# Optimization experiments

Hardware: AMD Instinct MI355X
Metric: run time of the kernel (lower is better)

## Reference

```python
import jax, jax.numpy as jnp
import numpy as np

D_MODEL = 256
D_INNER = 512
NHEADS = 8
HEADDIM = 64
NGROUPS = 1
D_DIST = 4
LOG_SCALE = 512.0
MAX_VALUE = 4.0
NUM_POINTS = 10
EPS = 1e-5


def roty(t):
    c, s = jnp.cos(t), jnp.sin(t)
    z, o = jnp.zeros_like(t), jnp.ones_like(t)
    r0 = jnp.stack([c, z, s], -1)
    r1 = jnp.stack([z, o, z], -1)
    r2 = jnp.stack([-s, z, c], -1)
    return jnp.stack([r0, r1, r2], -2)


def box_corners(center, size, angle):
    # flip_axis_to_camera: (x, -z, y)
    cam_c = jnp.stack([center[..., 0], -center[..., 2], center[..., 1]], -1)
    R = roty(angle)  # (B,K,3,3)
    sx = jnp.array([1, 1, -1, -1, 1, 1, -1, -1], jnp.float32)
    sy = jnp.array([1, 1, 1, 1, -1, -1, -1, -1], jnp.float32)
    sz = jnp.array([1, -1, -1, 1, 1, -1, -1, 1], jnp.float32)
    l, w, h = size[..., 0:1], size[..., 1:2], size[..., 2:3]
    local = jnp.stack([l * sx / 2, h * sy / 2, w * sz / 2], -1)  # (B,K,8,3)
    cam = jnp.einsum('bkcj,bkij->bkci', local, R) + cam_c[..., None, :]
    # camera -> lidar: (x, z, -y)
    return jnp.stack([cam[..., 0], cam[..., 2], -cam[..., 1]], -1)


def trilinear_sample(table, g):
    # table (P,P,P,C); g (N,3) normalized coords (gx,gy,gz); gx->axis2, gy->axis1, gz->axis0
    # replicates F.grid_sample(mode='bilinear', align_corners=False, padding_mode='zeros')
    P = table.shape[0]
    pix = ((g + 1.0) * P - 1.0) * 0.5
    k, j, i = pix[:, 0], pix[:, 1], pix[:, 2]
    i0f, j0f, k0f = jnp.floor(i), jnp.floor(j), jnp.floor(k)
    wi, wj, wk = i - i0f, j - j0f, k - k0f
    i0, j0, k0 = i0f.astype(jnp.int32), j0f.astype(jnp.int32), k0f.astype(jnp.int32)
    out = jnp.zeros((g.shape[0], table.shape[-1]), table.dtype)
    for a in (0, 1):
        for b in (0, 1):
            for c in (0, 1):
                ii, jj, kk = i0 + a, j0 + b, k0 + c
                valid = (ii >= 0) & (ii < P) & (jj >= 0) & (jj < P) & (kk >= 0) & (kk < P)
                v = table[jnp.clip(ii, 0, P - 1), jnp.clip(jj, 0, P - 1), jnp.clip(kk, 0, P - 1)]
                w = (wi if a else 1 - wi) * (wj if b else 1 - wj) * (wk if c else 1 - wk)
                out = out + jnp.where(valid, w, 0.0)[:, None] * v
    return out


def box_dist(key_xyz, query_xyz, query_size, query_angle, w1, b1, w2):
    B, K = query_xyz.shape[:2]
    L = key_xyz.shape[1]
    corners = jax.lax.stop_gradient(box_corners(query_xyz, query_size, query_angle))
    d = corners.reshape(B, K * 8, 3)[:, :, None, :] - key_xyz[:, None, :, :]  # (B,K*8,L,3)
    d = jnp.stack([d[..., 0], -d[..., 2], d[..., 1]], -1)
    R = roty(jnp.tile(query_angle, (1, 8)))  # matches torch .repeat((1,8)) ordering (bug-faithful)
    d = jnp.einsum('bqlj,bqjk->bqlk', d, R)
    d = jnp.stack([d[..., 0], d[..., 2], -d[..., 1]], -1)
    d = jnp.sign(d) * jnp.log2(jnp.abs(d) * LOG_SCALE + 1.0) / np.float32(np.log2(8.0))
    g = (d / MAX_VALUE).reshape(-1, 3)
    lin = jnp.linspace(-MAX_VALUE, MAX_VALUE, NUM_POINTS, dtype=jnp.float32)
    coords = jnp.stack(jnp.meshgrid(lin, lin, lin, indexing='ij'), -1)  # (P,P,P,3)
    table = jnp.maximum(coords @ w1.T + b1, 0.0) @ w2.T  # cpb MLP -> (P,P,P,4)
    samp = trilinear_sample(table, g).reshape(B, K, 8, L, D_DIST)
    return samp.sum(axis=2).transpose(0, 2, 1, 3)  # (B,L,K,4)


def dwconv7(x, w, b):
    # x (B,L,C), depthwise conv1d k=7 pad=3
    y = jax.lax.conv_general_dilated(jnp.swapaxes(x, 1, 2), w, (1,), [(3, 3)],
                                     dimension_numbers=('NCH', 'OIH', 'NCH'),
                                     feature_group_count=w.shape[0])
    return jnp.swapaxes(y + b[None, :, None], 1, 2)


def issm_scan(x, Bm, Cm, dt, A, h0):
    # x (B,L,H,hd), Bm/Cm (B,L,K), dt (B,L,K,H), h0 (B,H,hd,K); state index = query axis K
    dA = jnp.exp(dt * A)          # (B,L,K,H)
    dB = dt * Bm[..., None]       # (B,L,K,H)
    xs = (jnp.moveaxis(x, 1, 0), jnp.moveaxis(dA, 1, 0), jnp.moveaxis(dB, 1, 0), jnp.moveaxis(Cm, 1, 0))

    def step(h, inp):
        x_t, dA_t, dB_t, C_t = inp
        h = h * jnp.swapaxes(dA_t, 1, 2)[:, :, None, :] + x_t[..., None] * jnp.swapaxes(dB_t, 1, 2)[:, :, None, :]
        return h, jnp.einsum('bhdk,bk->bhd', h, C_t)

    hT, ys = jax.lax.scan(step, h0, xs)
    return jnp.moveaxis(ys, 0, 1), hT


def _forward(in_key, in_query, key_xyz, query_xyz, query_size, query_angle, Wkey, conv_w, conv_b, convb_w, convb_b, Wq, Wbc, Wdt, dt_bias, A_log, Dp, Wok, Woq, key_norm_w, ln_w, ln_b, cpb_w1, cpb_b1, cpb_w2):
    B, L, _ = in_key.shape
    K = in_query.shape[1]
    zxbcdt = in_key @ Wkey.T
    z = zxbcdt[..., :D_INNER]
    xbc = zxbcdt[..., D_INNER:2 * D_INNER + 2 * NGROUPS]
    dt_k = zxbcdt[..., 2 * D_INNER + 2 * NGROUPS:]
    xbc_f = jax.nn.silu(dwconv7(xbc, conv_w, conv_b))
    x = xbc_f[..., :D_INNER].reshape(B, L, NHEADS, HEADDIM)
    b_bias = xbc_f[..., D_INNER:D_INNER + NGROUPS]
    c_bias = xbc_f[..., D_INNER + NGROUPS:]
    xbc_b = jax.nn.silu(dwconv7(xbc_f, convb_w, convb_b))
    x_b = xbc_b[..., :D_INNER].reshape(B, L, NHEADS, HEADDIM)
    bb_b = xbc_b[..., D_INNER:D_INNER + NGROUPS]
    cb_b = xbc_b[..., D_INNER + NGROUPS:]
    dist = box_dist(key_xyz, query_xyz, query_size, query_angle, cpb_w1, cpb_b1, cpb_w2)  # (B,L,K,4)
    bc = dist @ Wbc.T  # (B,L,K,2*ngroups)
    Bm0, Cm0 = bc[..., 0], bc[..., 1]
    dt = jax.nn.softplus(dist @ Wdt.T + dt_k[:, :, None, :] + dt_bias)  # (B,L,K,H)
    A = -jnp.exp(A_log)
    h0 = (in_query @ Wq.T).reshape(B, K, NHEADS, HEADDIM).transpose(0, 2, 3, 1)  # (B,H,hd,K)
    y_f, h_f = issm_scan(x, Bm0 + b_bias, Cm0 + c_bias, dt, A, h0)
    rev = lambda a: jnp.flip(a, axis=1)
    y_b, h_b = issm_scan(rev(x_b), rev(Bm0 + bb_b), rev(Cm0 + cb_b), rev(dt), A, h0)
    y = y_f + rev(y_b) + Dp[None, None, :, None] * x
    yk = y.reshape(B, L, D_INNER)
    gated = yk * jax.nn.silu(z)
    gated = gated * jax.lax.rsqrt(jnp.mean(gated * gated, -1, keepdims=True) + EPS) * key_norm_w
    out_key = gated @ Wok.T
    state = (0.5 * (h_f + h_b)).transpose(0, 3, 1, 2).reshape(B, K, D_INNER)
    mu = jnp.mean(state, -1, keepdims=True)
    var = jnp.mean((state - mu) ** 2, -1, keepdims=True)
    out_query = (((state - mu) * jax.lax.rsqrt(var + EPS)) * ln_w + ln_b) @ Woq.T
    return out_key, out_query


def setup_inputs():
    key = jax.random.key(0)
    ks = jax.random.split(key, 24)
    B, L, K = 2, 1024, 128
    D, DI, H, G = D_MODEL, D_INNER, NHEADS, NGROUPS
    CC = DI + 2 * G
    n = jax.random.normal
    inp = {}
    inp['in_key'] = n(ks[0], (B, L, D), jnp.float32)
    inp['in_query'] = n(ks[1], (B, K, D), jnp.float32)
    inp['key_xyz'] = jax.random.uniform(ks[2], (B, L, 3))
    inp['query_xyz'] = jax.random.uniform(ks[3], (B, K, 3))
    inp['query_size'] = jax.random.uniform(ks[4], (B, K, 3)) + 0.1
    inp['query_angle'] = jax.random.uniform(ks[5], (B, K)) * 2.0 * np.float32(np.pi)
    inp['Wkey'] = n(ks[6], (2 * DI + 2 * G + H, D)) * 0.02
    inp['conv_w'] = n(ks[7], (CC, 1, 7)) * 0.1
    inp['conv_b'] = jnp.zeros((CC,))
    inp['convb_w'] = n(ks[8], (CC, 1, 7)) * 0.1
    inp['convb_b'] = jnp.zeros((CC,))
    inp['Wq'] = n(ks[9], (DI, D)) * 0.02
    inp['Wbc'] = n(ks[10], (2 * G, D_DIST)) * 0.1
    inp['Wdt'] = n(ks[11], (H, D_DIST)) * 0.1
    dt = jnp.exp(jax.random.uniform(ks[12], (H,)) * (np.float32(np.log(0.1)) - np.float32(np.log(1e-4))) + np.float32(np.log(1e-4)))
    inp['dt_bias'] = dt + jnp.log(-jnp.expm1(-dt))
    inp['A_log'] = jnp.log(jax.random.uniform(ks[13], (H,), minval=1.0, maxval=16.0))
    inp['Dp'] = jnp.ones((H,))
    inp['Wok'] = n(ks[14], (D, DI)) * 0.02
    inp['Woq'] = n(ks[15], (D, DI)) * 0.02
    inp['key_norm_w'] = jnp.ones((DI,))
    inp['ln_w'] = jnp.ones((DI,))
    inp['ln_b'] = jnp.zeros((DI,))
    inp['cpb_w1'] = n(ks[16], (128, 3)) * 0.1
    inp['cpb_b1'] = jnp.zeros((128,))
    inp['cpb_w2'] = n(ks[17], (D_DIST, 128)) * 0.1
    return inp


def reference(in_key, in_query, key_xyz, query_xyz, query_size, query_angle, Wkey, conv_w, conv_b, convb_w, convb_b, Wq, Wbc, Wdt, dt_bias, A_log, Dp, Wok, Woq, key_norm_w, ln_w, ln_b, cpb_w1, cpb_b1, cpb_w2):
    return _forward(in_key, in_query, key_xyz, query_xyz, query_size, query_angle, Wkey, conv_w, conv_b, convb_w, convb_b, Wq, Wbc, Wdt, dt_bias, A_log, Dp, Wok, Woq, key_norm_w, ln_w, ln_b, cpb_w1, cpb_b1, cpb_w2)
```

## Files before the change

kernel.cpp:

```cpp
#include <hip/hip_runtime.h>
#include <math.h>

#define B_ 2
#define L_ 1024
#define K_ 128
#define DM 256
#define DI 512
#define NH 8
#define HD 64
#define CC 514
#define ZCOLS 1034
#define NC 16
#define TC 64

__device__ __forceinline__ float wave_sum(float v) {
    v += __shfl_xor(v, 1);  v += __shfl_xor(v, 2);  v += __shfl_xor(v, 4);
    v += __shfl_xor(v, 8);  v += __shfl_xor(v, 16); v += __shfl_xor(v, 32);
    return v;
}

__device__ __forceinline__ float dpp_row_reduce16(float v) {
    int t;
    t = __builtin_amdgcn_update_dpp(0, __float_as_int(v), 0x128, 0xF, 0xF, true);
    v += __int_as_float(t);
    t = __builtin_amdgcn_update_dpp(0, __float_as_int(v), 0x124, 0xF, 0xF, true);
    v += __int_as_float(t);
    t = __builtin_amdgcn_update_dpp(0, __float_as_int(v), 0x122, 0xF, 0xF, true);
    v += __int_as_float(t);
    t = __builtin_amdgcn_update_dpp(0, __float_as_int(v), 0x121, 0xF, 0xF, true);
    v += __int_as_float(t);
    return v;
}

__device__ __forceinline__ float silu_f(float x) {
    return x / (1.f + expf(-x));
}

__device__ void gemm_dev(const float* __restrict__ A, const float* __restrict__ Bm,
                         float* __restrict__ C, int M, int N, int K, int bm, int bn) {
    __shared__ float As[2][16][68];
    __shared__ float Bs[2][16][68];
    const int tid = threadIdx.x;
    const int sr = tid >> 2;
    const int sk = (tid & 3) * 4;
    const int tx = tid & 15, ty = tid >> 4;
    const int NT = K >> 4;
    const float* Arow = A + (size_t)(bm + sr) * K + sk;
    const float* Brow = Bm + (size_t)(bn + sr) * K + sk;
    const bool bok = (bn + sr) < N;

    float4 av = *(const float4*)Arow;
    float4 bv = bok ? *(const float4*)Brow : make_float4(0.f, 0.f, 0.f, 0.f);
    As[0][sk + 0][sr] = av.x; As[0][sk + 1][sr] = av.y;
    As[0][sk + 2][sr] = av.z; As[0][sk + 3][sr] = av.w;
    Bs[0][sk + 0][sr] = bv.x; Bs[0][sk + 1][sr] = bv.y;
    Bs[0][sk + 2][sr] = bv.z; Bs[0][sk + 3][sr] = bv.w;
    __syncthreads();

    float acc[4][4] = {};
    for (int t = 0; t < NT; ++t) {
        if (t + 1 < NT) {
            av = *(const float4*)(Arow + (t + 1) * 16);
            bv = bok ? *(const float4*)(Brow + (t + 1) * 16) : make_float4(0.f, 0.f, 0.f, 0.f);
        }
        const int bi = t & 1;
#pragma unroll
        for (int kk = 0; kk < 16; ++kk) {
            float4 a = *(const float4*)&As[bi][kk][ty * 4];
            float4 b = *(const float4*)&Bs[bi][kk][tx * 4];
            acc[0][0] = fmaf(a.x, b.x, acc[0][0]); acc[0][1] = fmaf(a.x, b.y, acc[0][1]);
            acc[0][2] = fmaf(a.x, b.z, acc[0][2]); acc[0][3] = fmaf(a.x, b.w, acc[0][3]);
            acc[1][0] = fmaf(a.y, b.x, acc[1][0]); acc[1][1] = fmaf(a.y, b.y, acc[1][1]);
            acc[1][2] = fmaf(a.y, b.z, acc[1][2]); acc[1][3] = fmaf(a.y, b.w, acc[1][3]);
            acc[2][0] = fmaf(a.z, b.x, acc[2][0]); acc[2][1] = fmaf(a.z, b.y, acc[2][1]);
            acc[2][2] = fmaf(a.z, b.z, acc[2][2]); acc[2][3] = fmaf(a.z, b.w, acc[2][3]);
            acc[3][0] = fmaf(a.w, b.x, acc[3][0]); acc[3][1] = fmaf(a.w, b.y, acc[3][1]);
            acc[3][2] = fmaf(a.w, b.z, acc[3][2]); acc[3][3] = fmaf(a.w, b.w, acc[3][3]);
        }
        if (t + 1 < NT) {
            const int ni = (t + 1) & 1;
            As[ni][sk + 0][sr] = av.x; As[ni][sk + 1][sr] = av.y;
            As[ni][sk + 2][sr] = av.z; As[ni][sk + 3][sr] = av.w;
            Bs[ni][sk + 0][sr] = bv.x; Bs[ni][sk + 1][sr] = bv.y;
            Bs[ni][sk + 2][sr] = bv.z; Bs[ni][sk + 3][sr] = bv.w;
        }
        __syncthreads();
    }
#pragma unroll
    for (int i = 0; i < 4; ++i) {
        int m = bm + ty * 4 + i;
        int n0 = bn + tx * 4;
        if (n0 + 3 < N) {
            float* cp = &C[(size_t)m * N + n0];
            *(float2*)cp = make_float2(acc[i][0], acc[i][1]);
            *(float2*)(cp + 2) = make_float2(acc[i][2], acc[i][3]);
        } else {
#pragma unroll
            for (int j = 0; j < 4; ++j)
                if (n0 + j < N) C[(size_t)m * N + n0 + j] = acc[i][j];
        }
    }
}

__global__ __launch_bounds__(256, 4) void front_k(
    const float* __restrict__ in_key, const float* __restrict__ Wkey, float* __restrict__ zx,
    const float* __restrict__ in_query, const float* __restrict__ Wq, float* __restrict__ h0b,
    const float* __restrict__ qxyz, const float* __restrict__ qsize,
    const float* __restrict__ qang, const float* __restrict__ w1,
    const float* __restrict__ b1, const float* __restrict__ w2,
    float* __restrict__ cb, float* __restrict__ tbl) {
    int bid = blockIdx.x, tid = threadIdx.x;
    if (bid < 544) {
        gemm_dev(in_key, Wkey, zx, 2048, ZCOLS, 256, (bid & 31) * 64, (bid >> 5) * 64);
    } else if (bid < 576) {
        int r = bid - 544;
        gemm_dev(in_query, Wq, h0b, 256, 512, 256, (r & 3) * 64, (r >> 2) * 64);
    } else if (bid < 584) {
        int idx = (bid - 576) * 256 + tid;
        int b = idx >> 10;
        int q = idx & 1023;
        int k = q >> 3;
        int c = q & 7;
        const float sx[8] = {1, 1, -1, -1, 1, 1, -1, -1};
        const float sy[8] = {1, 1, 1, 1, -1, -1, -1, -1};
        const float sz[8] = {1, -1, -1, 1, 1, -1, -1, 1};
        float cx = qxyz[(b * K_ + k) * 3 + 0];
        float cy = qxyz[(b * K_ + k) * 3 + 1];
        float cz = qxyz[(b * K_ + k) * 3 + 2];
        float lv = qsize[(b * K_ + k) * 3 + 0];
        float wv = qsize[(b * K_ + k) * 3 + 1];
        float hv = qsize[(b * K_ + k) * 3 + 2];
        float ang = qang[b * K_ + k];
        float ca = cosf(ang), sa = sinf(ang);
        float ccx = cx, ccy = -cz, ccz = cy;
        float l0 = lv * sx[c] * 0.5f;
        float l1 = hv * sy[c] * 0.5f;
        float l2 = wv * sz[c] * 0.5f;
        float m0 = ca * l0 + sa * l2 + ccx;
        float m1 = l1 + ccy;
        float m2 = -sa * l0 + ca * l2 + ccz;
        float angr = qang[b * K_ + (q & (K_ - 1))];
        float4* o = (float4*)(cb + (size_t)idx * 8);
        o[0] = make_float4(m0, m2, -m1, cosf(angr));
        o[1] = make_float4(sinf(angr), 0.f, 0.f, 0.f);
    } else {
        int p = (bid - 584) * 256 + tid;
        if (p >= 1000) return;
        int i = p / 100, j = (p / 10) % 10, k = p % 10;
        float c0 = (8.f / 9.f) * i - 4.f;
        float c1 = (8.f / 9.f) * j - 4.f;
        float c2 = (8.f / 9.f) * k - 4.f;
        float a0 = 0.f, a1 = 0.f, a2 = 0.f, a3 = 0.f;
        for (int m = 0; m < 128; ++m) {
            float t = fmaf(c0, w1[m * 3 + 0], fmaf(c1, w1[m * 3 + 1], fmaf(c2, w1[m * 3 + 2], b1[m])));
            t = fmaxf(t, 0.f);
            a0 = fmaf(t, w2[m], a0);
            a1 = fmaf(t, w2[128 + m], a1);
            a2 = fmaf(t, w2[256 + m], a2);
            a3 = fmaf(t, w2[384 + m], a3);
        }
        tbl[p * 4 + 0] = a0; tbl[p * 4 + 1] = a1;
        tbl[p * 4 + 2] = a2; tbl[p * 4 + 3] = a3;
    }
}

__global__ void dwconv_silu(const float* __restrict__ xin, int in_stride, int in_off,
                            const float* __restrict__ w, const float* __restrict__ bias,
                            float* __restrict__ out) {
    int c = blockIdx.y * blockDim.x + threadIdx.x;
    if (c >= CC) return;
    int row0 = blockIdx.x * 2;
    int l0 = row0 & (L_ - 1);
    const float* xr = xin + (size_t)row0 * in_stride + in_off + c;
    float Lv[8];
#pragma unroll
    for (int i = 0; i < 8; ++i) {
        int ll = l0 + i - 3;
        Lv[i] = (ll >= 0 && ll < L_) ? xr[(ptrdiff_t)(i - 3) * in_stride] : 0.f;
    }
    float acc0 = bias[c], acc1 = bias[c];
#pragma unroll
    for (int j = 0; j < 7; ++j) {
        float wj = w[c * 7 + j];
        acc0 = fmaf(Lv[j], wj, acc0);
        acc1 = fmaf(Lv[j + 1], wj, acc1);
    }
    out[(size_t)row0 * CC + c] = silu_f(acc0);
    out[(size_t)(row0 + 1) * CC + c] = silu_f(acc1);
}

__global__ __launch_bounds__(128) void geo_k(
    const float* __restrict__ kxyz, const float* __restrict__ cb,
    const float* __restrict__ tbl, const float* __restrict__ zx,
    const float* __restrict__ xf, const float* __restrict__ xb,
    const float* __restrict__ wbc, const float* __restrict__ wdt,
    const float* __restrict__ dtb, const float* __restrict__ alog,
    float* __restrict__ dA, float* __restrict__ dBf, float* __restrict__ dBb,
    float* __restrict__ Cf, float* __restrict__ Cb) {
    __shared__ float t_s[4000];
    int row = blockIdx.x;
    int b = row >> 10;
    int l = row & 1023;
    int k = threadIdx.x;
    for (int i = threadIdx.x; i < 4000; i += 128) t_s[i] = tbl[i];
    __syncthreads();
    float kx = kxyz[(size_t)row * 3 + 0];
    float ky = kxyz[(size_t)row * 3 + 1];
    float kz = kxyz[(size_t)row * 3 + 2];
    float acc0 = 0.f, acc1 = 0.f, acc2 = 0.f, acc3 = 0.f;
#pragma unroll
    for (int c = 0; c < 8; ++c) {
        int q = k * 8 + c;
        const float4* p = (const float4*)(cb + (size_t)(b * 1024 + q) * 8);
        float4 v0 = p[0], v1 = p[1];
        float d0 = v0.x - kx, d1 = v0.y - ky, d2 = v0.z - kz;
        float rc = v0.w, rs = v1.x;
        float e0 = d0, e1 = -d2, e2 = d1;
        float f0 = rc * e0 - rs * e2;
        float f1 = e1;
        float f2 = rs * e0 + rc * e2;
        float g0 = f0, g1 = f2, g2 = -f1;
        g0 = copysignf(log2f(fabsf(g0) * 512.f + 1.f) * (1.f / 12.f), g0);
        g1 = copysignf(log2f(fabsf(g1) * 512.f + 1.f) * (1.f / 12.f), g1);
        g2 = copysignf(log2f(fabsf(g2) * 512.f + 1.f) * (1.f / 12.f), g2);
        float iq = 5.f * g2 + 4.5f;
        float jq = 5.f * g1 + 4.5f;
        float kq = 5.f * g0 + 4.5f;
        float i0f = floorf(iq), j0f = floorf(jq), k0f = floorf(kq);
        float wi = iq - i0f, wj = jq - j0f, wk = kq - k0f;
        int i0 = (int)i0f, j0 = (int)j0f, k0 = (int)k0f;
#pragma unroll
        for (int a = 0; a < 2; ++a) {
#pragma unroll
            for (int bb = 0; bb < 2; ++bb) {
#pragma unroll
                for (int cc = 0; cc < 2; ++cc) {
                    int ii = i0 + a, jj = j0 + bb, kk = k0 + cc;
                    if ((unsigned)ii < 10u && (unsigned)jj < 10u && (unsigned)kk < 10u) {
                        float wgt = (a ? wi : 1.f - wi) * (bb ? wj : 1.f - wj) * (cc ? wk : 1.f - wk);
                        const float* tp = &t_s[((ii * 10 + jj) * 10 + kk) * 4];
                        acc0 = fmaf(wgt, tp[0], acc0);
                        acc1 = fmaf(wgt, tp[1], acc1);
                        acc2 = fmaf(wgt, tp[2], acc2);
                        acc3 = fmaf(wgt, tp[3], acc3);
                    }
                }
            }
        }
    }
    float B0 = acc0 * wbc[0] + acc1 * wbc[1] + acc2 * wbc[2] + acc3 * wbc[3];
    float C0 = acc0 * wbc[4] + acc1 * wbc[5] + acc2 * wbc[6] + acc3 * wbc[7];
    float bbf = xf[(size_t)row * CC + 512], cbf = xf[(size_t)row * CC + 513];
    float bbb = xb[(size_t)row * CC + 512], cbb = xb[(size_t)row * CC + 513];
    Cf[(size_t)row * K_ + k] = C0 + cbf;
    Cb[(size_t)row * K_ + k] = C0 + cbb;
    float Bf = B0 + bbf, Bb = B0 + bbb;
#pragma unroll
    for (int hh = 0; hh < NH; ++hh) {
        float s = acc0 * wdt[hh * 4 + 0] + acc1 * wdt[hh * 4 + 1] +
                  acc2 * wdt[hh * 4 + 2] + acc3 * wdt[hh * 4 + 3];
        s += zx[(size_t)row * ZCOLS + 1026 + hh] + dtb[hh];
        float dtv = (s > 20.f) ? s : log1pf(expf(s));
        float Av = -expf(alog[hh]);
        size_t o = ((size_t)(b * NH + hh) * L_ + l) * K_ + k;
        dA[o] = expf(dtv * Av);
        dBf[o] = dtv * Bf;
        dBb[o] = dtv * Bb;
    }
}

__global__ __launch_bounds__(256) void scan_part6(
    const float* __restrict__ dA, const float* __restrict__ dBf, const float* __restrict__ dBb,
    const float* __restrict__ Cf, const float* __restrict__ Cb,
    const float* __restrict__ xf, const float* __restrict__ xb,
    float* __restrict__ Sbuf, float* __restrict__ Pbuf,
    float* __restrict__ yf, float* __restrict__ yb) {
    __shared__ float lds[2][3584];
    int bid = blockIdx.x;
    int c = bid & 15;
    int hh = (bid >> 4) & 7;
    int b = (bid >> 7) & 1;
    int dir = bid >> 8;
    int tid = threadIdx.x;
    int lane = tid & 63;
    int w = tid >> 6;
    int dg = lane >> 4, kg = lane & 15;
    int dloc = w * 4 + dg;
    int klo = kg * 4, khi = 64 + kg * 4;

    const float* Bsrc = dir ? dBb : dBf;
    const float* Csrc = dir ? Cb : Cf;
    const float* Xsrc = dir ? xb : xf;
    float* Ydst = dir ? yb : yf;
    int t0 = dir ? (L_ - 1 - c * TC) : c * TC;
    int stp = dir ? -1 : 1;

    const float* Abase = dA + ((size_t)(b * NH + hh) * L_) * K_;
    const float* Bbase = Bsrc + ((size_t)(b * NH + hh) * L_) * K_;
    const float* Cbase = Csrc + ((size_t)b * L_) * K_;
    const float* Xbase = Xsrc + ((size_t)b * L_) * CC + hh * HD;

    const bool hasx = (tid < 128);

    auto gaddr = [&](int v, int tb) -> const float* {
        if (v < 768) {
            int r = (v >> 5) & 7;
            int c4 = v & 31;
            int l = t0 + stp * (tb + r);
            const float* base = (v < 256) ? Abase : ((v < 512) ? Bbase : Cbase);
            return base + (size_t)l * K_ + c4 * 4;
        } else {
            int vv = v - 768;
            int r = vv >> 4, c4 = vv & 15;
            int l = t0 + stp * (tb + r);
            return Xbase + (size_t)l * CC + c4 * 4;
        }
    };

    float hA[8] = {0, 0, 0, 0, 0, 0, 0, 0};
    float hB[8] = {0, 0, 0, 0, 0, 0, 0, 0};
    float hC[8] = {0, 0, 0, 0, 0, 0, 0, 0};
    float hD[8] = {0, 0, 0, 0, 0, 0, 0, 0};
    float cum[8] = {1, 1, 1, 1, 1, 1, 1, 1};

    float4 rA = *(const float4*)gaddr(tid, 0);
    float4 rB = *(const float4*)gaddr(256 + tid, 0);
    float4 rC = *(const float4*)gaddr(512 + tid, 0);
    float4 rX = hasx ? *(const float4*)gaddr(768 + tid, 0) : make_float4(0, 0, 0, 0);
    *(float4*)&lds[0][4 * tid] = rA;
    *(float4*)&lds[0][1024 + 4 * tid] = rB;
    *(float4*)&lds[0][2048 + 4 * tid] = rC;
    if (hasx) *(float4*)&lds[0][3072 + 4 * tid] = rX;
    __syncthreads();

    float* pY = Ydst + ((size_t)(b * L_ + t0)) * DI + hh * HD + dloc;
    const ptrdiff_t dY = (ptrdiff_t)stp * DI;

    for (int it = 0; it < TC / 8; ++it) {
        int tb = it * 8;
        if (it < TC / 8 - 1) {
            rA = *(const float4*)gaddr(tid, tb + 8);
            rB = *(const float4*)gaddr(256 + tid, tb + 8);
            rC = *(const float4*)gaddr(512 + tid, tb + 8);
            if (hasx) rX = *(const float4*)gaddr(768 + tid, tb + 8);
        }
        const float* Lb = lds[it & 1];
        float4 aC0 = *(const float4*)&Lb[klo];
        float4 aC1 = *(const float4*)&Lb[khi];
        float4 bC0 = *(const float4*)&Lb[1024 + klo];
        float4 bC1 = *(const float4*)&Lb[1024 + khi];
        float4 cC0 = *(const float4*)&Lb[2048 + klo];
        float4 cC1 = *(const float4*)&Lb[2048 + khi];
        float x0 = Lb[3072 + dloc];
        float x1 = Lb[3072 + 16 + dloc];
        float x2 = Lb[3072 + 32 + dloc];
        float x3 = Lb[3072 + 48 + dloc];
        float4 aN0 = *(const float4*)&Lb[128 + klo];
        float4 aN1 = *(const float4*)&Lb[128 + khi];
        float4 bN0 = *(const float4*)&Lb[1024 + 128 + klo];
        float4 bN1 = *(const float4*)&Lb[1024 + 128 + khi];
#pragma unroll
        for (int st = 0; st < 8; ++st) {
            float4 aF0, aF1, bF0, bF1, cN0, cN1;
            float nx0 = 0.f, nx1 = 0.f, nx2 = 0.f, nx3 = 0.f;
            if (st < 6) {
                int o = (st + 2) * 128;
                aF0 = *(const float4*)&Lb[o + klo];
                aF1 = *(const float4*)&Lb[o + khi];
                bF0 = *(const float4*)&Lb[1024 + o + klo];
                bF1 = *(const float4*)&Lb[1024 + o + khi];
            }
            if (st < 7) {
                int o = (st + 1) * 128;
                cN0 = *(const float4*)&Lb[2048 + o + klo];
                cN1 = *(const float4*)&Lb[2048 + o + khi];
                int xo = 3072 + (st + 1) * 64 + dloc;
                nx0 = Lb[xo]; nx1 = Lb[xo + 16]; nx2 = Lb[xo + 32]; nx3 = Lb[xo + 48];
            }
            cum[0] *= aC0.x; cum[1] *= aC0.y; cum[2] *= aC0.z; cum[3] *= aC0.w;
            cum[4] *= aC1.x; cum[5] *= aC1.y; cum[6] *= aC1.z; cum[7] *= aC1.w;
            float u0, u1, u2, u3;
            hA[0] = fmaf(hA[0], aC0.x, x0 * bC0.x); u0 = hA[0] * cC0.x;
            hA[1] = fmaf(hA[1], aC0.y, x0 * bC0.y); u1 = hA[1] * cC0.y;
            hA[2] = fmaf(hA[2], aC0.z, x0 * bC0.z); u2 = hA[2] * cC0.z;
            hA[3] = fmaf(hA[3], aC0.w, x0 * bC0.w); u3 = hA[3] * cC0.w;
            hA[4] = fmaf(hA[4], aC1.x, x0 * bC1.x); u0 = fmaf(hA[4], cC1.x, u0);
            hA[5] = fmaf(hA[5], aC1.y, x0 * bC1.y); u1 = fmaf(hA[5], cC1.y, u1);
            hA[6] = fmaf(hA[6], aC1.z, x0 * bC1.z); u2 = fmaf(hA[6], cC1.z, u2);
            hA[7] = fmaf(hA[7], aC1.w, x0 * bC1.w); u3 = fmaf(hA[7], cC1.w, u3);
            float rrA = dpp_row_reduce16((u0 + u1) + (u2 + u3));
            hB[0] = fmaf(hB[0], aC0.x, x1 * bC0.x); u0 = hB[0] * cC0.x;
            hB[1] = fmaf(hB[1], aC0.y, x1 * bC0.y); u1 = hB[1] * cC0.y;
            hB[2] = fmaf(hB[2], aC0.z, x1 * bC0.z); u2 = hB[2] * cC0.z;
            hB[3] = fmaf(hB[3], aC0.w, x1 * bC0.w); u3 = hB[3] * cC0.w;
            hB[4] = fmaf(hB[4], aC1.x, x1 * bC1.x); u0 = fmaf(hB[4], cC1.x, u0);
            hB[5] = fmaf(hB[5], aC1.y, x1 * bC1.y); u1 = fmaf(hB[5], cC1.y, u1);
            hB[6] = fmaf(hB[6], aC1.z, x1 * bC1.z); u2 = fmaf(hB[6], cC1.z, u2);
            hB[7] = fmaf(hB[7], aC1.w, x1 * bC1.w); u3 = fmaf(hB[7], cC1.w, u3);
            float rrB = dpp_row_reduce16((u0 + u1) + (u2 + u3));
            hC[0] = fmaf(hC[0], aC0.x, x2 * bC0.x); u0 = hC[0] * cC0.x;
            hC[1] = fmaf(hC[1], aC0.y, x2 * bC0.y); u1 = hC[1] * cC0.y;
            hC[2] = fmaf(hC[2], aC0.z, x2 * bC0.z); u2 = hC[2] * cC0.z;
            hC[3] = fmaf(hC[3], aC0.w, x2 * bC0.w); u3 = hC[3] * cC0.w;
            hC[4] = fmaf(hC[4], aC1.x, x2 * bC1.x); u0 = fmaf(hC[4], cC1.x, u0);
            hC[5] = fmaf(hC[5], aC1.y, x2 * bC1.y); u1 = fmaf(hC[5], cC1.y, u1);
            hC[6] = fmaf(hC[6], aC1.z, x2 * bC1.z); u2 = fmaf(hC[6], cC1.z, u2);
            hC[7] = fmaf(hC[7], aC1.w, x2 * bC1.w); u3 = fmaf(hC[7], cC1.w, u3);
            float rrC = dpp_row_reduce16((u0 + u1) + (u2 + u3));
            hD[0] = fmaf(hD[0], aC0.x, x3 * bC0.x); u0 = hD[0] * cC0.x;
            hD[1] = fmaf(hD[1], aC0.y, x3 * bC0.y); u1 = hD[1] * cC0.y;
            hD[2] = fmaf(hD[2], aC0.z, x3 * bC0.z); u2 = hD[2] * cC0.z;
            hD[3] = fmaf(hD[3], aC0.w, x3 * bC0.w); u3 = hD[3] * cC0.w;
            hD[4] = fmaf(hD[4], aC1.x, x3 * bC1.x); u0 = fmaf(hD[4], cC1.x, u0);
            hD[5] = fmaf(hD[5], aC1.y, x3 * bC1.y); u1 = fmaf(hD[5], cC1.y, u1);
            hD[6] = fmaf(hD[6], aC1.z, x3 * bC1.z); u2 = fmaf(hD[6], cC1.z, u2);
            hD[7] = fmaf(hD[7], aC1.w, x3 * bC1.w); u3 = fmaf(hD[7], cC1.w, u3);
            float rrD = dpp_row_reduce16((u0 + u1) + (u2 + u3));
            if (kg == 0) { pY[0] = rrA; pY[16] = rrB; pY[32] = rrC; pY[48] = rrD; }
            pY += dY;
            if (st < 7) {
                aC0 = aN0; aC1 = aN1; bC0 = bN0; bC1 = bN1;
                cC0 = cN0; cC1 = cN1;
                x0 = nx0; x1 = nx1; x2 = nx2; x3 = nx3;
                if (st < 6) { aN0 = aF0; aN1 = aF1; bN0 = bF0; bN1 = bF1; }
            }
        }
        if (it < TC / 8 - 1) {
            *(float4*)&lds[(it + 1) & 1][4 * tid] = rA;
            *(float4*)&lds[(it + 1) & 1][1024 + 4 * tid] = rB;
            *(float4*)&lds[(it + 1) & 1][2048 + 4 * tid] = rC;
            if (hasx) *(float4*)&lds[(it + 1) & 1][3072 + 4 * tid] = rX;
        }
        __syncthreads();
    }

    int ibh = (dir * B_ + b) * NH + hh;
    {
        float* Sp = Sbuf + (((size_t)ibh * NC + c) * HD + dloc) * K_;
        *(float4*)(Sp + klo) = make_float4(hA[0], hA[1], hA[2], hA[3]);
        *(float4*)(Sp + khi) = make_float4(hA[4], hA[5], hA[6], hA[7]);
        Sp += (size_t)16 * K_;
        *(float4*)(Sp + klo) = make_float4(hB[0], hB[1], hB[2], hB[3]);
        *(float4*)(Sp + khi) = make_float4(hB[4], hB[5], hB[6], hB[7]);
        Sp += (size_t)16 * K_;
        *(float4*)(Sp + klo) = make_float4(hC[0], hC[1], hC[2], hC[3]);
        *(float4*)(Sp + khi) = make_float4(hC[4], hC[5], hC[6], hC[7]);
        Sp += (size_t)16 * K_;
        *(float4*)(Sp + klo) = make_float4(hD[0], hD[1], hD[2], hD[3]);
        *(float4*)(Sp + khi) = make_float4(hD[4], hD[5], hD[6], hD[7]);
    }
    if (dir == 0 && tid < 16) {
        float* Pp = Pbuf + ((size_t)((b * NH + hh) * NC + c)) * K_;
        *(float4*)(Pp + klo) = make_float4(cum[0], cum[1], cum[2], cum[3]);
        *(float4*)(Pp + khi) = make_float4(cum[4], cum[5], cum[6], cum[7]);
    }
}

__global__ __launch_bounds__(256) void scan_combine(
    const float* __restrict__ h0buf, float* __restrict__ Sbuf,
    const float* __restrict__ Pbuf, float* __restrict__ hfin) {
    int bid = blockIdx.x;
    int dq = bid & 3;
    int hh = (bid >> 2) & 7;
    int b = (bid >> 5) & 1;
    int dir = bid >> 6;
    int tid = threadIdx.x;
    int w = tid >> 6;
    int lane = tid & 63;
    int dsl = dq * 4 + w;
    int dg = lane >> 4, kg = lane & 15;
    int d = dsl * 4 + dg;
    int k0 = kg * 8;

    float H[8];
#pragma unroll
    for (int j = 0; j < 8; ++j)
        H[j] = h0buf[(size_t)(b * K_ + k0 + j) * DI + hh * HD + d];

    int ibh = (dir * B_ + b) * NH + hh;
    for (int c = 0; c < NC; ++c) {
        float* Sp = Sbuf + (((size_t)ibh * NC + c) * HD + d) * K_ + k0;
        int cF = dir ? (NC - 1 - c) : c;
        const float* Pp = Pbuf + ((size_t)((b * NH + hh) * NC + cF)) * K_ + k0;
        float4 sA = *(const float4*)(Sp + 0);
        float4 sB = *(const float4*)(Sp + 4);
        float4 pA = *(const float4*)(Pp + 0);
        float4 pB = *(const float4*)(Pp + 4);
        *(float4*)(Sp + 0) = make_float4(H[0], H[1], H[2], H[3]);
        *(float4*)(Sp + 4) = make_float4(H[4], H[5], H[6], H[7]);
        H[0] = fmaf(H[0], pA.x, sA.x); H[1] = fmaf(H[1], pA.y, sA.y);
        H[2] = fmaf(H[2], pA.z, sA.z); H[3] = fmaf(H[3], pA.w, sA.w);
        H[4] = fmaf(H[4], pB.x, sB.x); H[5] = fmaf(H[5], pB.y, sB.y);
        H[6] = fmaf(H[6], pB.z, sB.z); H[7] = fmaf(H[7], pB.w, sB.w);
    }
    float* hf = hfin + ((((size_t)dir * B_ + b) * NH + hh) * HD + d) * K_ + k0;
    *(float4*)(hf + 0) = make_float4(H[0], H[1], H[2], H[3]);
    *(float4*)(hf + 4) = make_float4(H[4], H[5], H[6], H[7]);
}

#define CP 72
#define WSWZ(k) ((((k) >> 3) & 3) << 2)
__global__ __launch_bounds__(256) void scan_corr(
    const float* __restrict__ dA, const float* __restrict__ Cf, const float* __restrict__ Cb,
    const float* __restrict__ Sbuf, float* __restrict__ yf, float* __restrict__ yb) {
    __shared__ float Wl[128][CP];
    __shared__ float Hl[128][CP];
    int iid = blockIdx.x;
    int c = iid & 15;
    int hh = (iid >> 4) & 7;
    int b = (iid >> 7) & 1;
    int dir = iid >> 8;
    int tid = threadIdx.x;
    const float* Csrc = dir ? Cb : Cf;

    if (tid < 128) {
        int k = tid;
        float cum = 1.f;
        const float* pA = dA + ((size_t)(b * NH + hh) * L_) * K_ + k;
        const float* pC = Csrc + ((size_t)b * L_) * K_ + k;
        int sw = WSWZ(k);
#pragma unroll 4
        for (int t = 0; t < TC; ++t) {
            int l = dir ? (L_ - 1 - (c * TC + t)) : (c * TC + t);
            cum *= pA[(size_t)l * K_];
            Wl[k][t ^ sw] = cum * pC[(size_t)l * K_];
        }
    }
    {
        int d = tid & 63, kq = tid >> 6;
        int ibh = (dir * B_ + b) * NH + hh;
        const float* Hp = Sbuf + (((size_t)ibh * NC + c) * HD + d) * K_;
#pragma unroll
        for (int i = 0; i < 8; ++i) {
            int q = kq * 8 + i;
            float4 v = *(const float4*)(Hp + q * 4);
            Hl[q * 4 + 0][d] = v.x; Hl[q * 4 + 1][d] = v.y;
            Hl[q * 4 + 2][d] = v.z; Hl[q * 4 + 3][d] = v.w;
        }
    }
    __syncthreads();
    int a = tid >> 4;
    int bc = tid & 15;
    int t0v = a * 4, d0v = bc * 4;
    float acc[4][4] = {};
    for (int k = 0; k < 128; ++k) {
        float4 w4 = *(const float4*)&Wl[k][t0v ^ WSWZ(k)];
        float4 h4 = *(const float4*)&Hl[k][d0v];
        acc[0][0] = fmaf(w4.x, h4.x, acc[0][0]); acc[0][1] = fmaf(w4.x, h4.y, acc[0][1]);
        acc[0][2] = fmaf(w4.x, h4.z, acc[0][2]); acc[0][3] = fmaf(w4.x, h4.w, acc[0][3]);
        acc[1][0] = fmaf(w4.y, h4.x, acc[1][0]); acc[1][1] = fmaf(w4.y, h4.y, acc[1][1]);
        acc[1][2] = fmaf(w4.y, h4.z, acc[1][2]); acc[1][3] = fmaf(w4.y, h4.w, acc[1][3]);
        acc[2][0] = fmaf(w4.z, h4.x, acc[2][0]); acc[2][1] = fmaf(w4.z, h4.y, acc[2][1]);
        acc[2][2] = fmaf(w4.z, h4.z, acc[2][2]); acc[2][3] = fmaf(w4.z, h4.w, acc[2][3]);
        acc[3][0] = fmaf(w4.w, h4.x, acc[3][0]); acc[3][1] = fmaf(w4.w, h4.y, acc[3][1]);
        acc[3][2] = fmaf(w4.w, h4.z, acc[3][2]); acc[3][3] = fmaf(w4.w, h4.w, acc[3][3]);
    }
    float* Ydst = dir ? yb : yf;
#pragma unroll
    for (int i = 0; i < 4; ++i) {
        int t = t0v + i;
        int l = dir ? (L_ - 1 - (c * TC + t)) : (c * TC + t);
        float* yp = Ydst + ((size_t)(b * L_ + l)) * DI + hh * HD + d0v;
        float4 old = *(float4*)yp;
        old.x += acc[i][0]; old.y += acc[i][1];
        old.z += acc[i][2]; old.w += acc[i][3];
        *(float4*)yp = old;
    }
}

__global__ __launch_bounds__(256) void gated_k(
    const float* __restrict__ yf, const float* __restrict__ yb,
    const float* __restrict__ xf, const float* __restrict__ zx,
    const float* __restrict__ Dp, const float* __restrict__ knw,
    float* __restrict__ gated) {
    __shared__ float sb[4];
    int row = blockIdx.x;
    int tid = threadIdx.x;
    float g[2];
    float ss = 0.f;
#pragma unroll
    for (int u = 0; u < 2; ++u) {
        int c = tid + u * 256;
        float yv = yf[(size_t)row * DI + c] + yb[(size_t)row * DI + c] +
                   Dp[c >> 6] * xf[(size_t)row * CC + c];
        float z = zx[(size_t)row * ZCOLS + c];
        float gv = yv * silu_f(z);
        g[u] = gv;
        ss = fmaf(gv, gv, ss);
    }
    float wsum = wave_sum(ss);
    if ((tid & 63) == 0) sb[tid >> 6] = wsum;
    __syncthreads();
    float tot = sb[0] + sb[1] + sb[2] + sb[3];
    float rms = rsqrtf(tot * (1.f / 512.f) + 1e-5f);
#pragma unroll
    for (int u = 0; u < 2; ++u) {
        int c = tid + u * 256;
        gated[(size_t)row * DI + c] = g[u] * rms * knw[c];
    }
}

__global__ __launch_bounds__(256) void final_k(
    const float* __restrict__ gated, const float* __restrict__ Wok, float* __restrict__ out,
    const float* __restrict__ hfin, const float* __restrict__ lnw,
    const float* __restrict__ lnb, const float* __restrict__ woq,
    float* __restrict__ outq) {
    int bid = blockIdx.x, tid = threadIdx.x;
    if (bid < 128) {
        gemm_dev(gated, Wok, out, 2048, 256, 512, (bid & 31) * 64, (bid >> 5) * 64);
        return;
    }
    __shared__ float sln[512];
    __shared__ float sb1[4];
    __shared__ float sb2[4];
    int bk = bid - 128;
    int b = bk >> 7;
    int k = bk & 127;
    float st[2];
    float ssum = 0.f;
#pragma unroll
    for (int u = 0; u < 2; ++u) {
        int c = tid + u * 256;
        int hh = c >> 6, d = c & 63;
        size_t o0 = (((size_t)(0 * B_ + b) * NH + hh) * HD + d) * K_ + k;
        size_t o1 = (((size_t)(1 * B_ + b) * NH + hh) * HD + d) * K_ + k;
        st[u] = 0.5f * (hfin[o0] + hfin[o1]);
        ssum += st[u];
    }
    float wsum = wave_sum(ssum);
    if ((tid & 63) == 0) sb1[tid >> 6] = wsum;
    __syncthreads();
    float mu = (sb1[0] + sb1[1] + sb1[2] + sb1[3]) * (1.f / 512.f);
    float vs = 0.f;
#pragma unroll
    for (int u = 0; u < 2; ++u) {
        float t = st[u] - mu;
        vs = fmaf(t, t, vs);
    }
    float wv = wave_sum(vs);
    if ((tid & 63) == 0) sb2[tid >> 6] = wv;
    __syncthreads();
    float var = (sb2[0] + sb2[1] + sb2[2] + sb2[3]) * (1.f / 512.f);
    float inv = rsqrtf(var + 1e-5f);
#pragma unroll
    for (int u = 0; u < 2; ++u) {
        int c = tid + u * 256;
        sln[c] = (st[u] - mu) * inv * lnw[c] + lnb[c];
    }
    __syncthreads();
    const float4* w4 = (const float4*)(woq + (size_t)tid * 512);
    float acc = 0.f;
#pragma unroll 4
    for (int i = 0; i < 128; ++i) {
        float4 wvv = w4[i];
        float4 sv = *(const float4*)&sln[i * 4];
        acc = fmaf(wvv.x, sv.x, acc);
        acc = fmaf(wvv.y, sv.y, acc);
        acc = fmaf(wvv.z, sv.z, acc);
        acc = fmaf(wvv.w, sv.w, acc);
    }
    outq[(size_t)bk * 256 + tid] = acc;
}

extern "C" void kernel_launch(void* const* d_in, const int* in_sizes, int n_in,
                              void* d_out, int out_size, void* d_ws, size_t ws_size,
                              hipStream_t stream) {
    const float* in_key      = (const float*)d_in[0];
    const float* in_query    = (const float*)d_in[1];
    const float* key_xyz     = (const float*)d_in[2];
    const float* query_xyz   = (const float*)d_in[3];
    const float* query_size  = (const float*)d_in[4];
    const float* query_angle = (const float*)d_in[5];
    const float* Wkey        = (const float*)d_in[6];
    const float* conv_w      = (const float*)d_in[7];
    const float* conv_b      = (const float*)d_in[8];
    const float* convb_w     = (const float*)d_in[9];
    const float* convb_b     = (const float*)d_in[10];
    const float* Wq          = (const float*)d_in[11];
    const float* Wbc         = (const float*)d_in[12];
    const float* Wdt         = (const float*)d_in[13];
    const float* dt_bias     = (const float*)d_in[14];
    const float* A_log       = (const float*)d_in[15];
    const float* Dp          = (const float*)d_in[16];
    const float* Wok         = (const float*)d_in[17];
    const float* Woq         = (const float*)d_in[18];
    const float* key_norm_w  = (const float*)d_in[19];
    const float* ln_w        = (const float*)d_in[20];
    const float* ln_b        = (const float*)d_in[21];
    const float* cpb_w1      = (const float*)d_in[22];
    const float* cpb_b1      = (const float*)d_in[23];
    const float* cpb_w2      = (const float*)d_in[24];
    float* out = (float*)d_out;

    float* wsf = (float*)d_ws;
    float* zx    = wsf + 0;
    float* xf    = wsf + 2117632;
    float* xb    = wsf + 3170304;
    float* tbl   = wsf + 4222976;
    float* cbuf  = wsf + 4226976;
    float* Pbuf  = wsf + 4243360;
    float* dAa   = wsf + 5291936;
    float* dBf   = wsf + 7389088;
    float* dBb   = wsf + 9486240;
    float* Cfb   = wsf + 11583392;
    float* Cbb   = wsf + 11845536;
    float* h0b   = wsf + 12107680;
    float* yfb   = wsf + 12238752;
    float* ybb   = wsf + 13287328;
    float* hfin  = wsf + 14335904;
    float* gated = wsf + 14598048;
    float* Sbuf  = wsf + 15646624;

    front_k<<<588, 256, 0, stream>>>(in_key, Wkey, zx, in_query, Wq, h0b,
                                     query_xyz, query_size, query_angle,
                                     cpb_w1, cpb_b1, cpb_w2, cbuf, tbl);
    dwconv_silu<<<dim3(1024, 3), 256, 0, stream>>>(zx, ZCOLS, 512, conv_w, conv_b, xf);
    dwconv_silu<<<dim3(1024, 3), 256, 0, stream>>>(xf, CC, 0, convb_w, convb_b, xb);
    geo_k<<<2048, 128, 0, stream>>>(key_xyz, cbuf, tbl, zx, xf, xb,
                                    Wbc, Wdt, dt_bias, A_log,
                                    dAa, dBf, dBb, Cfb, Cbb);
    scan_part6<<<512, 256, 0, stream>>>(dAa, dBf, dBb, Cfb, Cbb, xf, xb,
                                        Sbuf, Pbuf, yfb, ybb);
    scan_combine<<<128, 256, 0, stream>>>(h0b, Sbuf, Pbuf, hfin);
    scan_corr<<<512, 256, 0, stream>>>(dAa, Cfb, Cbb, Sbuf, yfb, ybb);
    gated_k<<<2048, 256, 0, stream>>>(yfb, ybb, xf, zx, Dp, key_norm_w, gated);
    final_k<<<384, 256, 0, stream>>>(gated, Wok, out, hfin, ln_w, ln_b, Woq,
                                     out + 524288);
}
```

Measured before the change: 193.9 us.

## Use bf16 MFMA for key projection GEMM with separate fp32 tail columns

Adds a conversion kernel that casts in_key and Wkey to bf16, then replaces the fp32 tiled GEMM for the key projection with a bf16 MFMA 16x16x32 path that loads operands straight from global memory. The last 8 output columns (1026..1033) are computed in fp32 by extra blocks, presumably to keep precision for the dt/BC columns. The aim is to cut the FP32 ALU cost of the largest GEMM. In exchange it adds a kernel launch and conversion traffic, and bf16 rounding of the main projection may affect accuracy.

Measured after the change: 179.4 us. 1.08x faster.

```diff
diff --git a/kernel.cpp b/kernel.cpp
--- a/kernel.cpp
+++ b/kernel.cpp
@@ -13,6 +13,9 @@
 #define NC 16
 #define TC 64
 
+typedef __attribute__((ext_vector_type(8))) short bf16x8;
+typedef __attribute__((ext_vector_type(4))) float f32x4;
+
 __device__ __forceinline__ float wave_sum(float v) {
     v += __shfl_xor(v, 1);  v += __shfl_xor(v, 2);  v += __shfl_xor(v, 4);
     v += __shfl_xor(v, 8);  v += __shfl_xor(v, 16); v += __shfl_xor(v, 32);
@@ -34,6 +37,32 @@
 
 __device__ __forceinline__ float silu_f(float x) {
     return x / (1.f + expf(-x));
+}
+
+__device__ __forceinline__ unsigned short f2bf(float f) {
+    unsigned u = __float_as_uint(f);
+    u = (u + 0x7FFFu + ((u >> 16) & 1u)) >> 16;
+    return (unsigned short)u;
+}
+
+__global__ __launch_bounds__(256) void cvt_k(const float* __restrict__ ik,
+                                             const float* __restrict__ wk,
+                                             unsigned short* __restrict__ ikb,
+                                             unsigned short* __restrict__ wkb) {
+    int i = blockIdx.x * 256 + threadIdx.x;
+    if (i < 131072) {
+        float4 v = ((const float4*)ik)[i];
+        ushort4 o;
+        o.x = f2bf(v.x); o.y = f2bf(v.y); o.z = f2bf(v.z); o.w = f2bf(v.w);
+        ((ushort4*)ikb)[i] = o;
+    } else {
+        int j = i - 131072;
+        if (j >= 69632) return;
+        float4 v = (j < 66176) ? ((const float4*)wk)[j] : make_float4(0.f, 0.f, 0.f, 0.f);
+        ushort4 o;
+        o.x = f2bf(v.x); o.y = f2bf(v.y); o.z = f2bf(v.z); o.w = f2bf(v.w);
+        ((ushort4*)wkb)[j] = o;
+    }
 }
 
 __device__ void gemm_dev(const float* __restrict__ A, const float* __restrict__ Bm,
@@ -103,7 +132,9 @@
 }
 
 __global__ __launch_bounds__(256, 4) void front_k(
-    const float* __restrict__ in_key, const float* __restrict__ Wkey, float* __restrict__ zx,
+    const unsigned short* __restrict__ ikb, const unsigned short* __restrict__ wkb,
+    const float* __restrict__ in_key, const float* __restrict__ Wkey,
+    float* __restrict__ zx,
     const float* __restrict__ in_query, const float* __restrict__ Wq, float* __restrict__ h0b,
     const float* __restrict__ qxyz, const float* __restrict__ qsize,
     const float* __restrict__ qang, const float* __restrict__ w1,
@@ -111,10 +142,40 @@
     float* __restrict__ cb, float* __restrict__ tbl) {
     int bid = blockIdx.x, tid = threadIdx.x;
     if (bid < 544) {
-        gemm_dev(in_key, Wkey, zx, 2048, ZCOLS, 256, (bid & 31) * 64, (bid >> 5) * 64);
+        int bm = (bid & 31) * 64, bn = (bid >> 5) * 64;
+        int lane = tid & 63, wv = tid >> 6;
+        int wm = wv >> 1, wn = wv & 1;
+        int r = lane & 15, kg = lane >> 4;
+        const unsigned short* A0 = ikb + (size_t)(bm + wm * 32 + r) * 256 + kg * 8;
+        const unsigned short* A1 = A0 + 16 * 256;
+        const unsigned short* B0 = wkb + (size_t)(bn + wn * 32 + r) * 256 + kg * 8;
+        const unsigned short* B1 = B0 + 16 * 256;
+        f32x4 acc00 = {0.f, 0.f, 0.f, 0.f}, acc01 = acc00, acc10 = acc00, acc11 = acc00;
+#pragma unroll
+        for (int k0 = 0; k0 < 256; k0 += 32) {
+            bf16x8 a0 = *(const bf16x8*)(A0 + k0);
+            bf16x8 a1 = *(const bf16x8*)(A1 + k0);
+            bf16x8 b0 = *(const bf16x8*)(B0 + k0);
+            bf16x8 b1 = *(const bf16x8*)(B1 + k0);
+            acc00 = __builtin_amdgcn_mfma_f32_16x16x32_bf16(a0, b0, acc00, 0, 0, 0);
+            acc01 = __builtin_amdgcn_mfma_f32_16x16x32_bf16(a0, b1, acc01, 0, 0, 0);
+            acc10 = __builtin_amdgcn_mfma_f32_16x16x32_bf16(a1, b0, acc10, 0, 0, 0);
+            acc11 = __builtin_amdgcn_mfma_f32_16x16x32_bf16(a1, b1, acc11, 0, 0, 0);
+        }
+        int mb = bm + wm * 32, nb = bn + wn * 32;
+#pragma unroll
+        for (int j = 0; j < 4; ++j) {
+            int m0 = mb + kg * 4 + j;
+            int n0 = nb + r;
+            if (n0 < 1026)      zx[(size_t)m0 * ZCOLS + n0] = acc00[j];
+            if (n0 + 16 < 1026) zx[(size_t)m0 * ZCOLS + n0 + 16] = acc01[j];
+            int m1 = m0 + 16;
+            if (n0 < 1026)      zx[(size_t)m1 * ZCOLS + n0] = acc10[j];
+            if (n0 + 16 < 1026) zx[(size_t)m1 * ZCOLS + n0 + 16] = acc11[j];
+        }
     } else if (bid < 576) {
-        int r = bid - 544;
-        gemm_dev(in_query, Wq, h0b, 256, 512, 256, (r & 3) * 64, (r >> 2) * 64);
+        int rr = bid - 544;
+        gemm_dev(in_query, Wq, h0b, 256, 512, 256, (rr & 3) * 64, (rr >> 2) * 64);
     } else if (bid < 584) {
         int idx = (bid - 576) * 256 + tid;
         int b = idx >> 10;
@@ -128,14 +189,14 @@
         float cy = qxyz[(b * K_ + k) * 3 + 1];
         float cz = qxyz[(b * K_ + k) * 3 + 2];
         float lv = qsize[(b * K_ + k) * 3 + 0];
-        float wv = qsize[(b * K_ + k) * 3 + 1];
+        float wv2 = qsize[(b * K_ + k) * 3 + 1];
         float hv = qsize[(b * K_ + k) * 3 + 2];
         float ang = qang[b * K_ + k];
         float ca = cosf(ang), sa = sinf(ang);
         float ccx = cx, ccy = -cz, ccz = cy;
         float l0 = lv * sx[c] * 0.5f;
         float l1 = hv * sy[c] * 0.5f;
-        float l2 = wv * sz[c] * 0.5f;
+        float l2 = wv2 * sz[c] * 0.5f;
         float m0 = ca * l0 + sa * l2 + ccx;
         float m1 = l1 + ccy;
         float m2 = -sa * l0 + ca * l2 + ccz;
@@ -143,7 +204,7 @@
         float4* o = (float4*)(cb + (size_t)idx * 8);
         o[0] = make_float4(m0, m2, -m1, cosf(angr));
         o[1] = make_float4(sinf(angr), 0.f, 0.f, 0.f);
-    } else {
+    } else if (bid < 588) {
         int p = (bid - 584) * 256 + tid;
         if (p >= 1000) return;
         int i = p / 100, j = (p / 10) % 10, k = p % 10;
@@ -161,6 +222,19 @@
         }
         tbl[p * 4 + 0] = a0; tbl[p * 4 + 1] = a1;
         tbl[p * 4 + 2] = a2; tbl[p * 4 + 3] = a3;
+    } else {
+        int row = (bid - 588) * 32 + (tid >> 3);
+        int colh = tid & 7;
+        const float* arow = in_key + (size_t)row * 256;
+        const float* wrow = Wkey + (size_t)(1026 + colh) * 256;
+        float acc = 0.f;
+#pragma unroll 8
+        for (int k = 0; k < 256; k += 4) {
+            float4 a = *(const float4*)(arow + k);
+            float4 wv2 = *(const float4*)(wrow + k);
+            acc = fmaf(a.x, wv2.x, fmaf(a.y, wv2.y, fmaf(a.z, wv2.z, fmaf(a.w, wv2.w, acc))));
+        }
+        zx[(size_t)row * ZCOLS + 1026 + colh] = acc;
     }
 }
 
@@ -710,8 +784,11 @@
     float* hfin  = wsf + 14335904;
     float* gated = wsf + 14598048;
     float* Sbuf  = wsf + 15646624;
-
-    front_k<<<588, 256, 0, stream>>>(in_key, Wkey, zx, in_query, Wq, h0b,
+    unsigned short* ikb = (unsigned short*)(wsf + 19840928);
+    unsigned short* wkb = (unsigned short*)(wsf + 20103072);
+
+    cvt_k<<<784, 256, 0, stream>>>(in_key, Wkey, ikb, wkb);
+    front_k<<<652, 256, 0, stream>>>(ikb, wkb, in_key, Wkey, zx, in_query, Wq, h0b,
                                      query_xyz, query_size, query_angle,
                                      cpb_w1, cpb_b1, cpb_w2, cbuf, tbl);
     dwconv_silu<<<dim3(1024, 3), 256, 0, stream>>>(zx, ZCOLS, 512, conv_w, conv_b, xf);
```
